# Kernel tuning notes

Measured on AMD Instinct MI355X. Metric: run time of the kernel, lower is better.

The kernel has to match this reference:

```python
import jax, jax.numpy as jnp
import numpy as np

B, CIN, L = 4, 128, 2048
D_MODEL, D_STATE, EXPAND, HEADDIM, NGROUPS = 256, 16, 3, 3, 1
D_INNER = EXPAND * D_MODEL            # 768
NHEADS = D_INNER // HEADDIM           # 256
CONV_DIM = D_INNER + 2 * NGROUPS * D_STATE   # 800
D_IN_PROJ = 2 * D_INNER + 2 * NGROUPS * D_STATE + NHEADS  # 1824
K_PROJ, D_CONV = 4, 4
EPS = 1e-5


def setup_inputs() -> dict:
    key = jax.random.key(0)
    ks = jax.random.split(key, 9)
    x = jax.random.normal(ks[0], (B, CIN, L), jnp.float32)
    proj_w = jax.random.normal(ks[1], (D_MODEL, CIN, K_PROJ), jnp.float32) / np.float32(np.sqrt(CIN * K_PROJ))
    in_proj_w = jax.random.normal(ks[2], (D_IN_PROJ, D_MODEL), jnp.float32) / np.float32(np.sqrt(D_MODEL))
    conv_w = jax.random.normal(ks[3], (CONV_DIM, 1, D_CONV), jnp.float32) / np.float32(np.sqrt(D_CONV))
    conv_b = jax.random.normal(ks[4], (CONV_DIM,), jnp.float32) * 0.01
    # dt_bias = inverse-softplus of dt ~ LogUniform[1e-3, 1e-1] (mamba2 init)
    u = jax.random.uniform(ks[5], (NHEADS,), jnp.float32)
    dt = jnp.exp(u * np.float32(np.log(0.1) - np.log(1e-3)) + np.float32(np.log(1e-3)))
    dt_bias = dt + jnp.log(-jnp.expm1(-dt))
    A_log = jnp.log(1.0 + 15.0 * jax.random.uniform(ks[6], (NHEADS,), jnp.float32))  # A in [-16,-1]
    D_skip = jnp.ones((NHEADS,), jnp.float32)
    norm_w = jnp.ones((D_INNER,), jnp.float32)
    out_proj_w = jax.random.normal(ks[7], (D_MODEL, D_INNER), jnp.float32) / np.float32(np.sqrt(D_INNER))
    return {"x": x, "proj_w": proj_w, "in_proj_w": in_proj_w, "conv_w": conv_w,
            "conv_b": conv_b, "dt_bias": dt_bias, "A_log": A_log, "D_skip": D_skip,
            "norm_w": norm_w, "out_proj_w": out_proj_w}


def _forward(x, proj_w, in_proj_w, conv_w, conv_b, dt_bias, A_log, D_skip, norm_w, out_proj_w):
    # outer Conv1d, padding='same' (k=4 -> left 1, right 2), no bias: (B,CIN,L)->(B,D_MODEL,L)
    h = jax.lax.conv_general_dilated(x, proj_w, (1,), [(1, 2)],
                                     dimension_numbers=("NCH", "OIH", "NCH"))
    u = h.transpose(0, 2, 1)                          # (B, L, d_model)
    zxbcdt = jnp.einsum("bld,ed->ble", u, in_proj_w)  # (B, L, 1824)
    z = zxbcdt[..., :D_INNER]                                     # (B,L,768)
    xBC = zxbcdt[..., D_INNER:D_INNER + CONV_DIM]                 # (B,L,800)
    dt = zxbcdt[..., D_INNER + CONV_DIM:]                         # (B,L,256)
    dt = jax.nn.softplus(dt + dt_bias)
    # depthwise causal conv (pad d_conv-1 on left) + SiLU
    xBC_c = jax.lax.conv_general_dilated(xBC.transpose(0, 2, 1), conv_w, (1,), [(D_CONV - 1, 0)],
                                         feature_group_count=CONV_DIM,
                                         dimension_numbers=("NCH", "OIH", "NCH"))
    xBC = jax.nn.silu(xBC_c + conv_b[None, :, None]).transpose(0, 2, 1)  # (B,L,800)
    xs = xBC[..., :D_INNER].reshape(B, L, NHEADS, HEADDIM)        # (B,L,H,P)
    Bm = xBC[..., D_INNER:D_INNER + D_STATE]                      # (B,L,N) (ngroups=1)
    Cm = xBC[..., D_INNER + D_STATE:]                             # (B,L,N)
    A = -jnp.exp(A_log)                                           # (H,)

    def step(hst, inp):
        dt_t, x_t, B_t, C_t = inp                 # (B,H),(B,H,P),(B,N),(B,N)
        dA = jnp.exp(dt_t * A)[:, :, None, None]  # (B,H,1,1)
        hst = dA * hst + jnp.einsum("bh,bhp,bn->bhpn", dt_t, x_t, B_t)
        y_t = jnp.einsum("bhpn,bn->bhp", hst, C_t)
        return hst, y_t

    h0 = jnp.zeros((B, NHEADS, HEADDIM, D_STATE), x.dtype)
    _, ys = jax.lax.scan(step, h0, (dt.transpose(1, 0, 2), xs.transpose(1, 0, 2, 3),
                                    Bm.transpose(1, 0, 2), Cm.transpose(1, 0, 2)))
    y = ys.transpose(1, 0, 2, 3) + D_skip[None, None, :, None] * xs   # (B,L,H,P)
    y = y.reshape(B, L, D_INNER)
    # gated RMSNorm: gate first, then normalize (norm_before_gate=False)
    y = y * jax.nn.silu(z)
    y = y * jax.lax.rsqrt(jnp.mean(y * y, axis=-1, keepdims=True) + EPS) * norm_w
    out = jnp.einsum("ble,de->bld", y, out_proj_w)   # (B,L,d_model)
    return out.transpose(0, 2, 1)                    # (B,d_model,L)


def reference(x, proj_w, in_proj_w, conv_w, conv_b, dt_bias, A_log, D_skip, norm_w, out_proj_w):
    return _forward(x, proj_w, in_proj_w, conv_w, conv_b, dt_bias, A_log, D_skip, norm_w, out_proj_w)
```

## Files before the change

kernel.cpp:

```cpp
#include <hip/hip_runtime.h>
#include <hip/hip_fp16.h>
#include <math.h>

#define B_     4
#define CIN    128
#define LEN    2048
#define DMODEL 256
#define DSTATE 16
#define NHEADS 256
#define DINNER 768
#define CONVDIM 800
#define DINPROJ 1824
#define EPS_   1e-5f
#define CHUNK  64
#define NCHUNK 32

typedef _Float16 f16x8 __attribute__((ext_vector_type(8)));
typedef float    f32x4 __attribute__((ext_vector_type(4)));

__device__ __forceinline__ float silu_(float x){ return x / (1.0f + __expf(-x)); }
__device__ __forceinline__ float softplus_(float x){
    return x > 0.f ? x + log1pf(__expf(-x)) : log1pf(__expf(x));
}

__device__ __forceinline__ void gl2lds16(const _Float16* g, _Float16* l){
    __builtin_amdgcn_global_load_lds(
        (const __attribute__((address_space(1))) void*)g,
        (__attribute__((address_space(3))) void*)l, 16, 0, 0);
}

__global__ __launch_bounds__(256) void k_f2h(const float* __restrict__ a,
                                             _Float16* __restrict__ o, int n){
    for (int i = blockIdx.x * 256 + threadIdx.x; i < n; i += gridDim.x * 256)
        o[i] = (_Float16)a[i];
}

__global__ __launch_bounds__(256) void k_im2col(const float* __restrict__ x,
                                                _Float16* __restrict__ xcol){
    __shared__ float xs[CIN][68];
    int blk = blockIdx.x;
    int b  = blk >> 5;
    int l0 = (blk & 31) << 6;
    const float* xb = x + (size_t)b * CIN * LEN;
    for (int idx = threadIdx.x; idx < CIN * 67; idx += 256){
        int ci = idx / 67, j = idx % 67;
        int gl = l0 - 1 + j;
        xs[ci][j] = (gl >= 0 && gl < LEN) ? xb[ci * LEN + gl] : 0.f;
    }
    __syncthreads();
    #pragma unroll
    for (int v = 0; v < 16; v++){
        int id = v * 256 + threadIdx.x;
        int rl = id >> 6, c = id & 63;
        f16x8 pk;
        #pragma unroll
        for (int e = 0; e < 8; e++){
            int ci = c * 2 + (e >> 2), k = e & 3;
            pk[e] = (_Float16)xs[ci][rl + k];
        }
        *(f16x8*)&xcol[((size_t)(b * LEN + l0 + rl)) * 512 + c * 8] = pk;
    }
}

template<int K, int EPI>
__global__ __launch_bounds__(256) void k_gemm(const _Float16* __restrict__ A,
                                              const _Float16* __restrict__ Bw,
                                              const float* __restrict__ dt_bias,
                                              _Float16* __restrict__ o_u,
                                              _Float16* __restrict__ o_z,
                                              _Float16* __restrict__ o_xbc,
                                              _Float16* __restrict__ o_dt,
                                              float* __restrict__ o_f){
    __shared__ __align__(16) _Float16 As[128 * 32];
    __shared__ __align__(16) _Float16 Bs[128 * 32];
    int tid  = threadIdx.x;
    int wv   = tid >> 6;
    int lane = tid & 63;
    int quad = lane >> 4;
    int l16  = lane & 15;
    int m0 = blockIdx.x * 128;
    int n0 = blockIdx.y * 128;
    int wm = (wv >> 1) * 64;
    int wn = (wv & 1) * 64;
    int srow = lane >> 2;
    int scol = (lane & 3) * 8;

    f32x4 acc[4][4];
    #pragma unroll
    for (int i = 0; i < 4; i++)
        #pragma unroll
        for (int j = 0; j < 4; j++)
            acc[i][j] = (f32x4){0.f, 0.f, 0.f, 0.f};

    for (int k0 = 0; k0 < K; k0 += 32){
        #pragma unroll
        for (int j = 0; j < 2; j++){
            int ar = m0 + wv * 32 + j * 16 + srow;
            gl2lds16(A + (size_t)ar * K + k0 + scol,
                     &As[(wv * 32 + j * 16) * 32]);
            int nr = n0 + wv * 32 + j * 16 + srow;
            if (EPI == 1) nr = nr > (DINPROJ - 1) ? (DINPROJ - 1) : nr;
            gl2lds16(Bw + (size_t)nr * K + k0 + scol,
                     &Bs[(wv * 32 + j * 16) * 32]);
        }
        __syncthreads();
        f16x8 af[4], bf[4];
        #pragma unroll
        for (int i = 0; i < 4; i++)
            af[i] = *(const f16x8*)&As[(wm + i * 16 + l16) * 32 + quad * 8];
        #pragma unroll
        for (int j = 0; j < 4; j++)
            bf[j] = *(const f16x8*)&Bs[(wn + j * 16 + l16) * 32 + quad * 8];
        #pragma unroll
        for (int i = 0; i < 4; i++)
            #pragma unroll
            for (int j = 0; j < 4; j++)
                acc[i][j] = __builtin_amdgcn_mfma_f32_16x16x32_f16(
                                af[i], bf[j], acc[i][j], 0, 0, 0);
        __syncthreads();
    }

    if (EPI == 0){
        #pragma unroll
        for (int j = 0; j < 4; j++){
            int col = n0 + wn + j * 16 + l16;
            #pragma unroll
            for (int i = 0; i < 4; i++){
                int row = m0 + wm + i * 16 + quad * 4;
                #pragma unroll
                for (int r = 0; r < 4; r++)
                    o_u[(size_t)(row + r) * DMODEL + col] = (_Float16)acc[i][j][r];
            }
        }
    } else if (EPI == 1){
        #pragma unroll
        for (int j = 0; j < 4; j++){
            int col = n0 + wn + j * 16 + l16;
            if (col < DINNER){
                #pragma unroll
                for (int i = 0; i < 4; i++){
                    int row = m0 + wm + i * 16 + quad * 4;
                    #pragma unroll
                    for (int r = 0; r < 4; r++)
                        o_z[(size_t)(row + r) * DINNER + col] = (_Float16)acc[i][j][r];
                }
            } else if (col < DINNER + CONVDIM){
                int cc = col - DINNER;
                #pragma unroll
                for (int i = 0; i < 4; i++){
                    int row = m0 + wm + i * 16 + quad * 4;
                    #pragma unroll
                    for (int r = 0; r < 4; r++)
                        o_xbc[(size_t)(row + r) * CONVDIM + cc] = (_Float16)acc[i][j][r];
                }
            } else if (col < DINPROJ){
                int hh = col - (DINNER + CONVDIM);
                float bias = dt_bias[hh];
                #pragma unroll
                for (int i = 0; i < 4; i++){
                    int row = m0 + wm + i * 16 + quad * 4;
                    #pragma unroll
                    for (int r = 0; r < 4; r++)
                        o_dt[(size_t)(row + r) * NHEADS + hh] =
                            (_Float16)softplus_(acc[i][j][r] + bias);
                }
            }
        }
    } else {
        #pragma unroll
        for (int i = 0; i < 4; i++){
            int row = m0 + wm + i * 16 + quad * 4;
            int b = row >> 11, l = row & (LEN - 1);
            #pragma unroll
            for (int j = 0; j < 4; j++){
                int d = n0 + wn + j * 16 + l16;
                *(f32x4*)&o_f[(((size_t)(b * DMODEL + d)) << 11) + l] = acc[i][j];
            }
        }
    }
}

__global__ __launch_bounds__(256) void k_dwconv(const __half* __restrict__ xbc,
                                                const float* __restrict__ cw,
                                                const float* __restrict__ cb,
                                                __half* __restrict__ xcc){
    int idx = blockIdx.x * 256 + threadIdx.x;
    int c = idx % CONVDIM;
    int r = idx / CONVDIM;
    int l = r & (LEN - 1);
    float4 wv = *(const float4*)(cw + c * 4);
    float acc = cb[c];
    if (l >= 3){
        const __half* base = xbc + (size_t)(r - 3) * CONVDIM + c;
        acc += __half2float(base[0]) * wv.x + __half2float(base[CONVDIM]) * wv.y +
               __half2float(base[2 * CONVDIM]) * wv.z + __half2float(base[3 * CONVDIM]) * wv.w;
    } else {
        const float wk[4] = {wv.x, wv.y, wv.z, wv.w};
        for (int k = 0; k < 4; k++){
            int t = l - 3 + k;
            if (t >= 0) acc += __half2float(xbc[(size_t)(r + k - 3) * CONVDIM + c]) * wk[k];
        }
    }
    xcc[idx] = __float2half(silu_(acc));
}

__global__ __launch_bounds__(64) void k_scanA(const __half* __restrict__ dtb,
                                              const __half* __restrict__ xcc,
                                              const float* __restrict__ A_log,
                                              __half* __restrict__ cstate,
                                              float* __restrict__ dsum){
    int blk = blockIdx.x;
    int c  = blk & (NCHUNK - 1);
    int hg = (blk >> 5) & 63;
    int b  = blk >> 11;
    int lane = threadIdx.x;
    int hl = lane >> 4;
    int n  = lane & 15;
    int h  = hg * 4 + hl;
    int c0 = h * 3;
    float A = -__expf(A_log[h]);
    int t0 = c * CHUNK;
    const __half* xr  = xcc + ((size_t)b * LEN + t0) * CONVDIM;
    const __half* dtp = dtb + ((size_t)b * LEN + t0) * NHEADS + h;
    float h0 = 0.f, h1 = 0.f, h2 = 0.f, sdt = 0.f;
    for (int t = 0; t < CHUNK; t++){
        float vx0 = __half2float(xr[c0]);
        float vx1 = __half2float(xr[c0 + 1]);
        float vx2 = __half2float(xr[c0 + 2]);
        float vB  = __half2float(xr[DINNER + n]);
        float cdt = __half2float(dtp[(size_t)t * NHEADS]);
        float dA  = __expf(cdt * A);
        float dtB = cdt * vB;
        h0 = fmaf(h0, dA, vx0 * dtB);
        h1 = fmaf(h1, dA, vx1 * dtB);
        h2 = fmaf(h2, dA, vx2 * dtB);
        sdt += cdt;
        xr += CONVDIM;
    }
    size_t sbase = (((size_t)(b * NHEADS + h)) * NCHUNK + c) * 48;
    cstate[sbase + n]      = __float2half(h0);
    cstate[sbase + 16 + n] = __float2half(h1);
    cstate[sbase + 32 + n] = __float2half(h2);
    if (n == 0) dsum[(size_t)(b * NHEADS + h) * NCHUNK + c] = __expf(A * sdt);
}

__global__ __launch_bounds__(64) void k_scanB(__half* __restrict__ cstate,
                                              const float* __restrict__ dsum){
    int bh = blockIdx.x;
    int lane = threadIdx.x;
    if (lane >= 48) return;
    __half* st = cstate + (size_t)bh * NCHUNK * 48 + lane;
    const float* dd = dsum + (size_t)bh * NCHUNK;
    float H = 0.f;
    for (int c = 0; c < NCHUNK; c++){
        float d = dd[c];
        float s = __half2float(st[(size_t)c * 48]);
        st[(size_t)c * 48] = __float2half(H);
        H = fmaf(H, d, s);
    }
}

__global__ __launch_bounds__(64) void k_scanC(const __half* __restrict__ dtb,
                                              const __half* __restrict__ xcc,
                                              const float* __restrict__ A_log,
                                              const float* __restrict__ D_skip,
                                              const __half* __restrict__ cstate,
                                              __half* __restrict__ y){
    int blk = blockIdx.x;
    int c  = blk & (NCHUNK - 1);
    int hg = (blk >> 5) & 63;
    int b  = blk >> 11;
    int lane = threadIdx.x;
    int hl = lane >> 4;
    int n  = lane & 15;
    int h  = hg * 4 + hl;
    int c0 = h * 3;
    float A   = -__expf(A_log[h]);
    float Dsk = D_skip[h];
    int t0 = c * CHUNK;
    const __half* xr  = xcc + ((size_t)b * LEN + t0) * CONVDIM;
    const __half* dtp = dtb + ((size_t)b * LEN + t0) * NHEADS + h;
    size_t sbase = (((size_t)(b * NHEADS + h)) * NCHUNK + c) * 48;
    float h0 = __half2float(cstate[sbase + n]);
    float h1 = __half2float(cstate[sbase + 16 + n]);
    float h2 = __half2float(cstate[sbase + 32 + n]);
    __half* yp = y + ((size_t)b * LEN + t0) * DINNER + c0;
    for (int t = 0; t < CHUNK; t++){
        float vx0 = __half2float(xr[c0]);
        float vx1 = __half2float(xr[c0 + 1]);
        float vx2 = __half2float(xr[c0 + 2]);
        float vB  = __half2float(xr[DINNER + n]);
        float vC  = __half2float(xr[DINNER + DSTATE + n]);
        float cdt = __half2float(dtp[(size_t)t * NHEADS]);
        float dA  = __expf(cdt * A);
        float dtB = cdt * vB;
        h0 = fmaf(h0, dA, vx0 * dtB);
        h1 = fmaf(h1, dA, vx1 * dtB);
        h2 = fmaf(h2, dA, vx2 * dtB);
        float p0 = h0 * vC, p1 = h1 * vC, p2 = h2 * vC;
        #pragma unroll
        for (int m = 1; m < 16; m <<= 1){
            p0 += __shfl_xor(p0, m, 64);
            p1 += __shfl_xor(p1, m, 64);
            p2 += __shfl_xor(p2, m, 64);
        }
        if (n < 3){
            float pv = (n == 0) ? p0 : ((n == 1) ? p1 : p2);
            float xv = (n == 0) ? vx0 : ((n == 1) ? vx1 : vx2);
            yp[n] = __float2half(fmaf(Dsk, xv, pv));
        }
        xr += CONVDIM;
        yp += DINNER;
    }
}

__global__ __launch_bounds__(256) void k_norm(__half* __restrict__ y,
                                              const __half* __restrict__ z,
                                              const float* __restrict__ nw){
    __shared__ float wsum[4];
    size_t r = blockIdx.x;
    int tid = threadIdx.x;
    const __half* zr = z + r * DINNER;
    __half* yr = y + r * DINNER;
    int e0 = tid, e1 = tid + 256, e2 = tid + 512;
    float t0 = __half2float(yr[e0]) * silu_(__half2float(zr[e0]));
    float t1 = __half2float(yr[e1]) * silu_(__half2float(zr[e1]));
    float t2 = __half2float(yr[e2]) * silu_(__half2float(zr[e2]));
    float ss = t0 * t0 + t1 * t1 + t2 * t2;
    #pragma unroll
    for (int m = 1; m < 64; m <<= 1) ss += __shfl_xor(ss, m, 64);
    if ((tid & 63) == 0) wsum[tid >> 6] = ss;
    __syncthreads();
    float tot = wsum[0] + wsum[1] + wsum[2] + wsum[3];
    float sc = rsqrtf(tot / (float)DINNER + EPS_);
    yr[e0] = __float2half(t0 * sc * nw[e0]);
    yr[e1] = __float2half(t1 * sc * nw[e1]);
    yr[e2] = __float2half(t2 * sc * nw[e2]);
}

extern "C" void kernel_launch(void* const* d_in, const int* in_sizes, int n_in,
                              void* d_out, int out_size, void* d_ws, size_t ws_size,
                              hipStream_t stream) {
    const float* x          = (const float*)d_in[0];
    const float* proj_w     = (const float*)d_in[1];
    const float* in_proj_w  = (const float*)d_in[2];
    const float* conv_w     = (const float*)d_in[3];
    const float* conv_b     = (const float*)d_in[4];
    const float* dt_bias    = (const float*)d_in[5];
    const float* A_log      = (const float*)d_in[6];
    const float* D_skip     = (const float*)d_in[7];
    const float* norm_w     = (const float*)d_in[8];
    const float* out_proj_w = (const float*)d_in[9];
    float* out = (float*)d_out;

    char* ob = (char*)d_out;
    _Float16* pw_h  = (_Float16*)ob;
    _Float16* ipw_h = (_Float16*)(ob + 262144);

    char* wsb = (char*)d_ws;
    _Float16* xcol  = (_Float16*)(wsb);
    _Float16* u_h   = (_Float16*)(wsb + 8388608);
    __half*   xcc_h = (__half*)(wsb);
    __half*   z_h   = (__half*)(wsb + 13107200);
    __half*   xbc_h = (__half*)(wsb + 25690112);
    __half*   y_h   = xbc_h;
    __half*   dt_h  = (__half*)(wsb + 38797312);
    __half*   cstate= (__half*)(wsb + 42991616);
    float*    dsum  = (float*)(wsb + 46137344);
    _Float16* opw_h = (_Float16*)(wsb + 46268416);

    k_f2h   <<<64, 256, 0, stream>>>(proj_w,     pw_h,  DMODEL * CIN * 4);
    k_f2h   <<<64, 256, 0, stream>>>(in_proj_w,  ipw_h, DINPROJ * DMODEL);
    k_f2h   <<<64, 256, 0, stream>>>(out_proj_w, opw_h, DMODEL * DINNER);
    k_im2col<<<128, 256, 0, stream>>>(x, xcol);
    k_gemm<512, 0><<<dim3(64, 2), 256, 0, stream>>>(xcol, pw_h, nullptr,
        u_h, nullptr, nullptr, nullptr, nullptr);
    k_gemm<256, 1><<<dim3(64, 15), 256, 0, stream>>>(u_h, ipw_h, dt_bias,
        nullptr, (_Float16*)z_h, (_Float16*)xbc_h, (_Float16*)dt_h, nullptr);
    k_dwconv<<<25600, 256, 0, stream>>>(xbc_h, conv_w, conv_b, xcc_h);
    k_scanA <<<8192, 64, 0, stream>>>(dt_h, xcc_h, A_log, cstate, dsum);
    k_scanB <<<1024, 64, 0, stream>>>(cstate, dsum);
    k_scanC <<<8192, 64, 0, stream>>>(dt_h, xcc_h, A_log, D_skip, cstate, y_h);
    k_norm  <<<8192, 256, 0, stream>>>(y_h, z_h, norm_w);
    k_gemm<768, 2><<<dim3(64, 2), 256, 0, stream>>>((const _Float16*)y_h, opw_h,
        nullptr, nullptr, nullptr, nullptr, nullptr, out);
}
```

Measured before the change: 318.4 us.

## Replace sequential chunk scans with SSD-style intra-band matmul and fused inter-band correction

```diff
diff --git a/kernel.cpp b/kernel.cpp
--- a/kernel.cpp
+++ b/kernel.cpp
@@ -12,10 +12,11 @@
 #define CONVDIM 800
 #define DINPROJ 1824
 #define EPS_   1e-5f
-#define CHUNK  64
-#define NCHUNK 32
+#define BAND   64
+#define NBAND  32
 
 typedef _Float16 f16x8 __attribute__((ext_vector_type(8)));
+typedef _Float16 f16x4 __attribute__((ext_vector_type(4)));
 typedef float    f32x4 __attribute__((ext_vector_type(4)));
 
 __device__ __forceinline__ float silu_(float x){ return x / (1.0f + __expf(-x)); }
@@ -204,44 +205,228 @@
     xcc[idx] = __float2half(silu_(acc));
 }
 
-__global__ __launch_bounds__(64) void k_scanA(const __half* __restrict__ dtb,
+__global__ __launch_bounds__(256, 3) void k_y(const __half* __restrict__ dtb,
                                               const __half* __restrict__ xcc,
                                               const float* __restrict__ A_log,
+                                              __half* __restrict__ y,
+                                              float* __restrict__ E0,
                                               __half* __restrict__ cstate,
                                               float* __restrict__ dsum){
-    int blk = blockIdx.x;
-    int c  = blk & (NCHUNK - 1);
-    int hg = (blk >> 5) & 63;
-    int b  = blk >> 11;
-    int lane = threadIdx.x;
-    int hl = lane >> 4;
-    int n  = lane & 15;
-    int h  = hg * 4 + hl;
-    int c0 = h * 3;
-    float A = -__expf(A_log[h]);
-    int t0 = c * CHUNK;
-    const __half* xr  = xcc + ((size_t)b * LEN + t0) * CONVDIM;
-    const __half* dtp = dtb + ((size_t)b * LEN + t0) * NHEADS + h;
-    float h0 = 0.f, h1 = 0.f, h2 = 0.f, sdt = 0.f;
-    for (int t = 0; t < CHUNK; t++){
-        float vx0 = __half2float(xr[c0]);
-        float vx1 = __half2float(xr[c0 + 1]);
-        float vx2 = __half2float(xr[c0 + 2]);
-        float vB  = __half2float(xr[DINNER + n]);
-        float cdt = __half2float(dtp[(size_t)t * NHEADS]);
-        float dA  = __expf(cdt * A);
-        float dtB = cdt * vB;
-        h0 = fmaf(h0, dA, vx0 * dtB);
-        h1 = fmaf(h1, dA, vx1 * dtB);
-        h2 = fmaf(h2, dA, vx2 * dtB);
-        sdt += cdt;
-        xr += CONVDIM;
-    }
-    size_t sbase = (((size_t)(b * NHEADS + h)) * NCHUNK + c) * 48;
-    cstate[sbase + n]      = __float2half(h0);
-    cstate[sbase + 16 + n] = __float2half(h1);
-    cstate[sbase + 32 + n] = __float2half(h2);
-    if (n == 0) dsum[(size_t)(b * NHEADS + h) * NCHUNK + c] = __expf(A * sdt);
+    __shared__ __align__(16) char smem[45056];
+    __half* sBC = (__half*)smem;
+    __half* sX  = (__half*)(smem + 5120);
+    float*  sG  = (float*)(smem + 18432);
+    float*  sD  = (float*)(smem + 22528);
+    __half* sDT = (__half*)(smem + 31744);
+    __half* sHL = (__half*)(smem + 35840);
+
+    int band = blockIdx.x, hg = blockIdx.y, b = blockIdx.z;
+    int row0 = band * BAND;
+    int tid = threadIdx.x;
+    int wv = tid >> 6, lane = tid & 63;
+
+    {
+        int row = tid >> 2, off = tid & 3;
+        f16x8 v = *(const f16x8*)((const char*)xcc +
+                    (size_t)(b * LEN + row0 + row) * 1600 + 1536 + off * 16);
+        *(f16x8*)&sBC[row * 40 + off * 8] = v;
+    }
+    #pragma unroll
+    for (int i = 0; i < 3; i++){
+        int c = tid + i * 256;
+        int row = c / 12, off = c % 12;
+        f16x8 v = *(const f16x8*)((const char*)xcc +
+                    (size_t)(b * LEN + row0 + row) * 1600 + hg * 192 + off * 16);
+        *(f16x8*)&sX[row * 104 + off * 8] = v;
+    }
+    gl2lds16((const _Float16*)((const char*)dtb +
+               (size_t)(b * LEN + row0 + (tid >> 2)) * 512 + hg * 64 + (lane & 3) * 16),
+             (_Float16*)(smem + 31744 + wv * 1024));
+    __syncthreads();
+
+    {
+        int h = tid & 31;
+        float A = -__expf(A_log[hg * 32 + h]);
+        #pragma unroll
+        for (int i = 0; i < 8; i++){
+            int t = (tid >> 5) + i * 8;
+            sD[t * 36 + h] = __expf(A * __half2float(sDT[t * 32 + h]));
+        }
+    }
+    __syncthreads();
+
+    if (tid < 32){
+        int h = tid;
+        float E = 1.f;
+        float* ep = E0 + ((size_t)(b * LEN + row0)) * 256 + hg * 32 + h;
+        for (int t = 0; t < 64; t++){
+            E *= sD[t * 36 + h];
+            *ep = E;
+            ep += 256;
+        }
+        dsum[(size_t)(b * 256 + hg * 32 + h) * NBAND + band] = E;
+    } else if (tid < 160){
+        int base = (tid - 32) * 8;
+        int tt = base >> 4;
+        f16x8 ca = *(const f16x8*)&sBC[tt * 40 + 16];
+        f16x8 cb = *(const f16x8*)&sBC[tt * 40 + 24];
+        float cf[16];
+        #pragma unroll
+        for (int n = 0; n < 16; n++) cf[n] = (n < 8) ? (float)ca[n] : (float)cb[n - 8];
+        #pragma unroll
+        for (int j = 0; j < 8; j++){
+            int idx = base + j;
+            int t2 = idx >> 4, ss = idx & 15;
+            if (t2 != tt){
+                tt = t2;
+                ca = *(const f16x8*)&sBC[tt * 40 + 16];
+                cb = *(const f16x8*)&sBC[tt * 40 + 24];
+                #pragma unroll
+                for (int n = 0; n < 16; n++) cf[n] = (n < 8) ? (float)ca[n] : (float)cb[n - 8];
+            }
+            int s = (tt & 48) + ss;
+            f16x8 ba = *(const f16x8*)&sBC[s * 40];
+            f16x8 bb = *(const f16x8*)&sBC[s * 40 + 8];
+            float acc = 0.f;
+            #pragma unroll
+            for (int n = 0; n < 8; n++)
+                acc += cf[n] * (float)ba[n] + cf[n + 8] * (float)bb[n];
+            sG[tt * 16 + ss] = acc;
+        }
+    } else {
+        for (int idx = tid - 160; idx < 2048; idx += 96){
+            int t = idx >> 5, h = idx & 31;
+            float dtv = __half2float(sDT[t * 32 + h]);
+            int xi = t * 104 + h * 3;
+            sX[xi]     = (_Float16)((float)sX[xi]     * dtv);
+            sX[xi + 1] = (_Float16)((float)sX[xi + 1] * dtv);
+            sX[xi + 2] = (_Float16)((float)sX[xi + 2] * dtv);
+        }
+    }
+    __syncthreads();
+
+    int t = tid >> 2, hsub = tid & 3, Hb = hsub * 8;
+    int tmod = t & 15, tseg = t & 48;
+    float w[8], y0[8], y1[8], y2[8];
+    #pragma unroll
+    for (int i = 0; i < 8; i++){ w[i] = 1.f; y0[i] = 0.f; y1[i] = 0.f; y2[i] = 0.f; }
+
+    for (int d = 0; d <= tmod; d++){
+        int s = t - d;
+        float g = sG[t * 16 + (tmod - d)];
+        f32x4 Dv0 = *(const f32x4*)&sD[s * 36 + Hb];
+        f32x4 Dv1 = *(const f32x4*)&sD[s * 36 + Hb + 4];
+        f16x8 xv0 = *(const f16x8*)&sX[s * 104 + hsub * 24];
+        f16x8 xv1 = *(const f16x8*)&sX[s * 104 + hsub * 24 + 8];
+        f16x8 xv2 = *(const f16x8*)&sX[s * 104 + hsub * 24 + 16];
+        #define XV(i) ((i) < 8 ? (float)xv0[(i)] : ((i) < 16 ? (float)xv1[(i)-8] : (float)xv2[(i)-16]))
+        #pragma unroll
+        for (int hh = 0; hh < 8; hh++){
+            float wg = w[hh] * g;
+            y0[hh] = fmaf(wg, XV(hh * 3 + 0), y0[hh]);
+            y1[hh] = fmaf(wg, XV(hh * 3 + 1), y1[hh]);
+            y2[hh] = fmaf(wg, XV(hh * 3 + 2), y2[hh]);
+            w[hh] *= (hh < 4) ? Dv0[hh] : Dv1[hh - 4];
+        }
+        #undef XV
+    }
+
+    if (tid < 128){
+        int h2 = tid >> 2, ng = tid & 3;
+        float hc[12];
+        #pragma unroll
+        for (int i = 0; i < 12; i++) hc[i] = 0.f;
+        for (int k = 0; k < 4; k++){
+            float F[12];
+            #pragma unroll
+            for (int i = 0; i < 12; i++) F[i] = 0.f;
+            float v = 1.f;
+            for (int ss = 15; ss >= 0; ss--){
+                int s = k * 16 + ss;
+                float x0 = (float)sX[s * 104 + h2 * 3];
+                float x1 = (float)sX[s * 104 + h2 * 3 + 1];
+                float x2 = (float)sX[s * 104 + h2 * 3 + 2];
+                f16x4 bv = *(const f16x4*)&sBC[s * 40 + ng * 4];
+                #pragma unroll
+                for (int nn = 0; nn < 4; nn++){
+                    float wb = v * (float)bv[nn];
+                    F[nn * 3 + 0] = fmaf(wb, x0, F[nn * 3 + 0]);
+                    F[nn * 3 + 1] = fmaf(wb, x1, F[nn * 3 + 1]);
+                    F[nn * 3 + 2] = fmaf(wb, x2, F[nn * 3 + 2]);
+                }
+                v *= sD[s * 36 + h2];
+            }
+            #pragma unroll
+            for (int i = 0; i < 12; i++) hc[i] = fmaf(v, hc[i], F[i]);
+            if (k < 3){
+                __half* hp = &sHL[(k * 32 + h2) * 48 + ng * 12];
+                #pragma unroll
+                for (int q = 0; q < 3; q++){
+                    f16x4 pk;
+                    #pragma unroll
+                    for (int e = 0; e < 4; e++) pk[e] = (_Float16)hc[q * 4 + e];
+                    *(f16x4*)&hp[q * 4] = pk;
+                }
+            } else {
+                __half* cp = cstate + ((size_t)((b * 256 + hg * 32 + h2) * NBAND + band)) * 48 + ng * 12;
+                #pragma unroll
+                for (int q = 0; q < 3; q++){
+                    f16x4 pk;
+                    #pragma unroll
+                    for (int e = 0; e < 4; e++) pk[e] = (_Float16)hc[q * 4 + e];
+                    *(f16x4*)&cp[q * 4] = pk;
+                }
+            }
+        }
+    }
+    __syncthreads();
+
+    {
+        f16x8 cva = *(const f16x8*)&sBC[t * 40 + 16];
+        f16x8 cvb = *(const f16x8*)&sBC[t * 40 + 24];
+        float cf[16];
+        #pragma unroll
+        for (int n = 0; n < 16; n++) cf[n] = (n < 8) ? (float)cva[n] : (float)cvb[n - 8];
+        int k = t >> 4;
+        if (k > 0){
+            #pragma unroll
+            for (int hh = 0; hh < 8; hh++){
+                int h = Hb + hh;
+                const __half* hl = &sHL[((k - 1) * 32 + h) * 48];
+                f16x8 hv0 = *(const f16x8*)&hl[0];
+                f16x8 hv1 = *(const f16x8*)&hl[8];
+                f16x8 hv2 = *(const f16x8*)&hl[16];
+                f16x8 hv3 = *(const f16x8*)&hl[24];
+                f16x8 hv4 = *(const f16x8*)&hl[32];
+                f16x8 hv5 = *(const f16x8*)&hl[40];
+                #define HV(i) ((i)<8?(float)hv0[(i)]:(i)<16?(float)hv1[(i)-8]:(i)<24?(float)hv2[(i)-16]:\
+                               (i)<32?(float)hv3[(i)-24]:(i)<40?(float)hv4[(i)-32]:(float)hv5[(i)-40])
+                float a0 = 0.f, a1 = 0.f, a2 = 0.f;
+                #pragma unroll
+                for (int n = 0; n < 16; n++){
+                    a0 = fmaf(cf[n], HV(n * 3 + 0), a0);
+                    a1 = fmaf(cf[n], HV(n * 3 + 1), a1);
+                    a2 = fmaf(cf[n], HV(n * 3 + 2), a2);
+                }
+                #undef HV
+                y0[hh] = fmaf(w[hh], a0, y0[hh]);
+                y1[hh] = fmaf(w[hh], a1, y1[hh]);
+                y2[hh] = fmaf(w[hh], a2, y2[hh]);
+            }
+        }
+        __half* yp = y + (size_t)(b * LEN + row0 + t) * DINNER + hg * 96 + hsub * 24;
+        #pragma unroll
+        for (int c = 0; c < 3; c++){
+            f16x8 pk;
+            #pragma unroll
+            for (int e2 = 0; e2 < 8; e2++){
+                int gi = c * 8 + e2;
+                int hh = gi / 3, p = gi % 3;
+                pk[e2] = (_Float16)(p == 0 ? y0[hh] : (p == 1 ? y1[hh] : y2[hh]));
+            }
+            *(f16x8*)&yp[c * 8] = pk;
+        }
+    }
 }
 
 __global__ __launch_bounds__(64) void k_scanB(__half* __restrict__ cstate,
@@ -249,10 +434,10 @@
     int bh = blockIdx.x;
     int lane = threadIdx.x;
     if (lane >= 48) return;
-    __half* st = cstate + (size_t)bh * NCHUNK * 48 + lane;
-    const float* dd = dsum + (size_t)bh * NCHUNK;
+    __half* st = cstate + (size_t)bh * NBAND * 48 + lane;
+    const float* dd = dsum + (size_t)bh * NBAND;
     float H = 0.f;
-    for (int c = 0; c < NCHUNK; c++){
+    for (int c = 0; c < NBAND; c++){
         float d = dd[c];
         float s = __half2float(st[(size_t)c * 48]);
         st[(size_t)c * 48] = __float2half(H);
@@ -260,82 +445,62 @@
     }
 }
 
-__global__ __launch_bounds__(64) void k_scanC(const __half* __restrict__ dtb,
-                                              const __half* __restrict__ xcc,
-                                              const float* __restrict__ A_log,
-                                              const float* __restrict__ D_skip,
-                                              const __half* __restrict__ cstate,
-                                              __half* __restrict__ y){
-    int blk = blockIdx.x;
-    int c  = blk & (NCHUNK - 1);
-    int hg = (blk >> 5) & 63;
-    int b  = blk >> 11;
-    int lane = threadIdx.x;
-    int hl = lane >> 4;
-    int n  = lane & 15;
-    int h  = hg * 4 + hl;
-    int c0 = h * 3;
-    float A   = -__expf(A_log[h]);
-    float Dsk = D_skip[h];
-    int t0 = c * CHUNK;
-    const __half* xr  = xcc + ((size_t)b * LEN + t0) * CONVDIM;
-    const __half* dtp = dtb + ((size_t)b * LEN + t0) * NHEADS + h;
-    size_t sbase = (((size_t)(b * NHEADS + h)) * NCHUNK + c) * 48;
-    float h0 = __half2float(cstate[sbase + n]);
-    float h1 = __half2float(cstate[sbase + 16 + n]);
-    float h2 = __half2float(cstate[sbase + 32 + n]);
-    __half* yp = y + ((size_t)b * LEN + t0) * DINNER + c0;
-    for (int t = 0; t < CHUNK; t++){
-        float vx0 = __half2float(xr[c0]);
-        float vx1 = __half2float(xr[c0 + 1]);
-        float vx2 = __half2float(xr[c0 + 2]);
-        float vB  = __half2float(xr[DINNER + n]);
-        float vC  = __half2float(xr[DINNER + DSTATE + n]);
-        float cdt = __half2float(dtp[(size_t)t * NHEADS]);
-        float dA  = __expf(cdt * A);
-        float dtB = cdt * vB;
-        h0 = fmaf(h0, dA, vx0 * dtB);
-        h1 = fmaf(h1, dA, vx1 * dtB);
-        h2 = fmaf(h2, dA, vx2 * dtB);
-        float p0 = h0 * vC, p1 = h1 * vC, p2 = h2 * vC;
-        #pragma unroll
-        for (int m = 1; m < 16; m <<= 1){
-            p0 += __shfl_xor(p0, m, 64);
-            p1 += __shfl_xor(p1, m, 64);
-            p2 += __shfl_xor(p2, m, 64);
-        }
-        if (n < 3){
-            float pv = (n == 0) ? p0 : ((n == 1) ? p1 : p2);
-            float xv = (n == 0) ? vx0 : ((n == 1) ? vx1 : vx2);
-            yp[n] = __float2half(fmaf(Dsk, xv, pv));
-        }
-        xr += CONVDIM;
-        yp += DINNER;
-    }
-}
-
 __global__ __launch_bounds__(256) void k_norm(__half* __restrict__ y,
                                               const __half* __restrict__ z,
+                                              const __half* __restrict__ xcc,
+                                              const float* __restrict__ E0,
+                                              const __half* __restrict__ cstate,
+                                              const float* __restrict__ D_skip,
                                               const float* __restrict__ nw){
+    __shared__ __align__(16) char nsm[24576 + 64];
+    __half* sHI = (__half*)nsm;
+    float*  sCf = (float*)(nsm + 24576);
     __shared__ float wsum[4];
-    size_t r = blockIdx.x;
+    int r = blockIdx.x;
+    int b = r >> 11, l = r & (LEN - 1), band = l >> 6;
     int tid = threadIdx.x;
-    const __half* zr = z + r * DINNER;
-    __half* yr = y + r * DINNER;
-    int e0 = tid, e1 = tid + 256, e2 = tid + 512;
-    float t0 = __half2float(yr[e0]) * silu_(__half2float(zr[e0]));
-    float t1 = __half2float(yr[e1]) * silu_(__half2float(zr[e1]));
-    float t2 = __half2float(yr[e2]) * silu_(__half2float(zr[e2]));
-    float ss = t0 * t0 + t1 * t1 + t2 * t2;
+    int wv = tid >> 6, lane = tid & 63;
+
+    #pragma unroll
+    for (int i = 0; i < 6; i++){
+        int chunk = (wv + i * 4) * 64 + lane;
+        int head = chunk / 6, off = chunk % 6;
+        gl2lds16((const _Float16*)((const char*)cstate +
+                   ((size_t)(b * 256 + head) * NBAND + band) * 96 + off * 16),
+                 (_Float16*)(nsm + (wv + i * 4) * 1024));
+    }
+    if (tid < 16)
+        sCf[tid] = __half2float(xcc[(size_t)r * CONVDIM + DINNER + DSTATE + tid]);
+    __syncthreads();
+
+    const __half* zr = z + (size_t)r * DINNER;
+    const __half* xr = xcc + (size_t)r * CONVDIM;
+    const float*  er = E0 + (size_t)r * 256;
+    __half* yr = y + (size_t)r * DINNER;
+    float tv[3];
+    #pragma unroll
+    for (int q = 0; q < 3; q++){
+        int e = tid + q * 256;
+        int h = e / 3, p = e - h * 3;
+        float corr = 0.f;
+        #pragma unroll
+        for (int n = 0; n < 16; n++)
+            corr = fmaf(sCf[n], __half2float(sHI[h * 48 + n * 3 + p]), corr);
+        float yf = __half2float(yr[e]) + er[h] * corr + D_skip[h] * __half2float(xr[e]);
+        tv[q] = yf * silu_(__half2float(zr[e]));
+    }
+    float ss = tv[0] * tv[0] + tv[1] * tv[1] + tv[2] * tv[2];
     #pragma unroll
     for (int m = 1; m < 64; m <<= 1) ss += __shfl_xor(ss, m, 64);
     if ((tid & 63) == 0) wsum[tid >> 6] = ss;
     __syncthreads();
     float tot = wsum[0] + wsum[1] + wsum[2] + wsum[3];
     float sc = rsqrtf(tot / (float)DINNER + EPS_);
-    yr[e0] = __float2half(t0 * sc * nw[e0]);
-    yr[e1] = __float2half(t1 * sc * nw[e1]);
-    yr[e2] = __float2half(t2 * sc * nw[e2]);
+    #pragma unroll
+    for (int q = 0; q < 3; q++){
+        int e = tid + q * 256;
+        yr[e] = __float2half(tv[q] * sc * nw[e]);
+    }
 }
 
 extern "C" void kernel_launch(void* const* d_in, const int* in_sizes, int n_in,
@@ -356,6 +521,7 @@
     char* ob = (char*)d_out;
     _Float16* pw_h  = (_Float16*)ob;
     _Float16* ipw_h = (_Float16*)(ob + 262144);
+    float*    E0    = (float*)d_out;
 
     char* wsb = (char*)d_ws;
     _Float16* xcol  = (_Float16*)(wsb);
@@ -378,10 +544,10 @@
     k_gemm<256, 1><<<dim3(64, 15), 256, 0, stream>>>(u_h, ipw_h, dt_bias,
         nullptr, (_Float16*)z_h, (_Float16*)xbc_h, (_Float16*)dt_h, nullptr);
     k_dwconv<<<25600, 256, 0, stream>>>(xbc_h, conv_w, conv_b, xcc_h);
-    k_scanA <<<8192, 64, 0, stream>>>(dt_h, xcc_h, A_log, cstate, dsum);
+    k_y     <<<dim3(NBAND, 8, B_), 256, 0, stream>>>(dt_h, xcc_h, A_log,
+                                                     y_h, E0, cstate, dsum);
     k_scanB <<<1024, 64, 0, stream>>>(cstate, dsum);
-    k_scanC <<<8192, 64, 0, stream>>>(dt_h, xcc_h, A_log, D_skip, cstate, y_h);
-    k_norm  <<<8192, 256, 0, stream>>>(y_h, z_h, norm_w);
+    k_norm  <<<8192, 256, 0, stream>>>(y_h, z_h, xcc_h, E0, cstate, D_skip, norm_w);
     k_gemm<768, 2><<<dim3(64, 2), 256, 0, stream>>>((const _Float16*)y_h, opw_h,
         nullptr, nullptr, nullptr, nullptr, nullptr, out);
 }
```

New measurement: 326.5 us. 1.03x slower.
